# Kernel tuning notes

Measured on AMD Instinct MI355X. Metric: run time of the kernel, lower is better.

Reference implementation:

```python
import jax, jax.numpy as jnp
import numpy as np

EPS = 0.0  # GIN epsilon (train_eps=False)

def setup_inputs() -> dict:
    key = jax.random.key(0)
    k_x, k_e, k_w1, k_w2 = jax.random.split(key, 4)
    N, E, D = 100000, 625000, 128
    x = jax.random.normal(k_x, (N, D), dtype=jnp.float32)
    edge_index = jax.random.randint(k_e, (2, E), 0, N, dtype=jnp.int32)
    s = 1.0 / np.sqrt(D)
    W1 = jax.random.normal(k_w1, (D, D), dtype=jnp.float32) * s
    b1 = jnp.zeros((D,), dtype=jnp.float32)
    W2 = jax.random.normal(k_w2, (D, D), dtype=jnp.float32) * s
    b2 = jnp.zeros((D,), dtype=jnp.float32)
    return {"x": x, "edge_index": edge_index, "W1": W1, "b1": b1, "W2": W2, "b2": b2}

def reference(x, edge_index, W1, b1, W2, b2):
    # GINConv: out_i = MLP((1+eps)*x_i + sum_{j in N(i)} x_j)
    src = edge_index[0]
    dst = edge_index[1]
    agg = jax.ops.segment_sum(x[src], dst, num_segments=x.shape[0])  # [N, D]
    h = (1.0 + EPS) * x + agg
    # MLP: Linear -> ReLU -> Dropout(eval: identity) -> Linear
    h = jax.nn.relu(h @ W1.T + b1)
    h = h @ W2.T + b2
    # outer activation; outer dropout is identity in eval
    return jax.nn.relu(h)
```

## Files before the change

### kernel.cpp

```cpp
#include <hip/hip_runtime.h>


#define D 128
#define HLD 136
#define KSLOT 32
#define CSTR 32

typedef __attribute__((ext_vector_type(8))) short bf16x8;
typedef __attribute__((ext_vector_type(4))) float f32x4;

__device__ __forceinline__ short f2bf(float f) {
    union { float f; unsigned u; } v; v.f = f;
    unsigned r = v.u + 0x7fffu + ((v.u >> 16) & 1u);
    return (short)(r >> 16);
}
__device__ __forceinline__ float bflo(unsigned u) {
    union { unsigned u; float f; } v; v.u = u << 16; return v.f;
}
__device__ __forceinline__ float bfhi(unsigned u) {
    union { unsigned u; float f; } v; v.u = u & 0xffff0000u; return v.f;
}
__device__ __forceinline__ unsigned pack2(float a, float b) {
    return ((unsigned)(unsigned short)f2bf(a)) | (((unsigned)(unsigned short)f2bf(b)) << 16);
}

__global__ __launch_bounds__(256) void convert_fill(const float4* __restrict__ x4,
                                                    unsigned short* __restrict__ xb,
                                                    const int* __restrict__ ei,
                                                    int* __restrict__ cnt,
                                                    int* __restrict__ bucket,
                                                    int nConv, int nConvBlocks, int E) {
    if ((int)blockIdx.x < nConvBlocks) {
        int t = blockIdx.x * 256 + threadIdx.x;
        if (t < nConv) {
            float4 a = x4[2 * t], b = x4[2 * t + 1];
            bf16x8 r;
            r[0] = f2bf(a.x); r[1] = f2bf(a.y); r[2] = f2bf(a.z); r[3] = f2bf(a.w);
            r[4] = f2bf(b.x); r[5] = f2bf(b.y); r[6] = f2bf(b.z); r[7] = f2bf(b.w);
            ((bf16x8*)xb)[t] = r;
        }
    } else {
        int t4 = ((int)blockIdx.x - nConvBlocks) * 256 + threadIdx.x;
        int E4 = E >> 2;
        if (t4 < E4) {
            const int4* ei4 = (const int4*)ei;
            int4 s = ei4[t4];
            int4 d = ei4[E4 + t4];
            int sl;
            sl = atomicAdd(&cnt[d.x * CSTR], 1); if (sl < KSLOT) bucket[d.x * KSLOT + sl] = s.x;
            sl = atomicAdd(&cnt[d.y * CSTR], 1); if (sl < KSLOT) bucket[d.y * KSLOT + sl] = s.y;
            sl = atomicAdd(&cnt[d.z * CSTR], 1); if (sl < KSLOT) bucket[d.z * KSLOT + sl] = s.z;
            sl = atomicAdd(&cnt[d.w * CSTR], 1); if (sl < KSLOT) bucket[d.w * KSLOT + sl] = s.w;
        }
    }
}

__global__ __launch_bounds__(256) void gather_kernel(const uint4* __restrict__ xb4,
                                                     const int* __restrict__ cnt,
                                                     const int* __restrict__ bucket,
                                                     uint4* __restrict__ h04, int N) {
    int g = blockIdx.x * 256 + threadIdx.x;
    int node = g >> 4;
    if (node >= N) return;
    int lane = g & 15;
    int deg = cnt[node * CSTR];
    deg = deg < KSLOT ? deg : KSLOT;
    const int bb = node * KSLOT;

    uint4 sv = xb4[node * 16 + lane];
    float a0 = bflo(sv.x), a1 = bfhi(sv.x), a2 = bflo(sv.y), a3 = bfhi(sv.y);
    float a4 = bflo(sv.z), a5 = bfhi(sv.z), a6 = bflo(sv.w), a7 = bfhi(sv.w);

    int e = 0;
    for (; e + 3 < deg; e += 4) {
        int s0 = bucket[bb + e], s1 = bucket[bb + e + 1];
        int s2 = bucket[bb + e + 2], s3 = bucket[bb + e + 3];
        uint4 p0 = xb4[s0 * 16 + lane];
        uint4 p1 = xb4[s1 * 16 + lane];
        uint4 p2 = xb4[s2 * 16 + lane];
        uint4 p3 = xb4[s3 * 16 + lane];
        a0 += bflo(p0.x) + bflo(p1.x) + bflo(p2.x) + bflo(p3.x);
        a1 += bfhi(p0.x) + bfhi(p1.x) + bfhi(p2.x) + bfhi(p3.x);
        a2 += bflo(p0.y) + bflo(p1.y) + bflo(p2.y) + bflo(p3.y);
        a3 += bfhi(p0.y) + bfhi(p1.y) + bfhi(p2.y) + bfhi(p3.y);
        a4 += bflo(p0.z) + bflo(p1.z) + bflo(p2.z) + bflo(p3.z);
        a5 += bfhi(p0.z) + bfhi(p1.z) + bfhi(p2.z) + bfhi(p3.z);
        a6 += bflo(p0.w) + bflo(p1.w) + bflo(p2.w) + bflo(p3.w);
        a7 += bfhi(p0.w) + bfhi(p1.w) + bfhi(p2.w) + bfhi(p3.w);
    }
    for (; e < deg; ++e) {
        uint4 p = xb4[bucket[bb + e] * 16 + lane];
        a0 += bflo(p.x); a1 += bfhi(p.x); a2 += bflo(p.y); a3 += bfhi(p.y);
        a4 += bflo(p.z); a5 += bfhi(p.z); a6 += bflo(p.w); a7 += bfhi(p.w);
    }
    uint4 r;
    r.x = pack2(a0, a1);
    r.y = pack2(a2, a3);
    r.z = pack2(a4, a5);
    r.w = pack2(a6, a7);
    h04[node * 16 + lane] = r;
}

__global__ __launch_bounds__(512) void mlp_fused(const short* __restrict__ h0,
                                                 const float* __restrict__ W1,
                                                 const float* __restrict__ b1,
                                                 const float* __restrict__ W2,
                                                 const float* __restrict__ b2,
                                                 float* __restrict__ out, int N) {
    __shared__ short W1l[D * HLD];
    __shared__ short W2l[D * HLD];
    __shared__ short h1l[D * HLD];

    {
        const float4* W14 = (const float4*)W1;
        const float4* W24 = (const float4*)W2;
        for (int idx = threadIdx.x; idx < D * (D / 4); idx += 512) {
            int n = idx >> 5;
            int k4 = idx & 31;
            float4 w = W14[idx];
            short* dp = &W1l[n * HLD + k4 * 4];
            dp[0] = f2bf(w.x); dp[1] = f2bf(w.y); dp[2] = f2bf(w.z); dp[3] = f2bf(w.w);
            w = W24[idx];
            dp = &W2l[n * HLD + k4 * 4];
            dp[0] = f2bf(w.x); dp[1] = f2bf(w.y); dp[2] = f2bf(w.z); dp[3] = f2bf(w.w);
        }
    }
    __syncthreads();

    const int wave = threadIdx.x >> 6;
    const int lane = threadIdx.x & 63;
    const int m = lane & 15;
    const int quad = lane >> 4;
    const int tiles = (N + 127) / 128;

    for (int t = blockIdx.x; t < tiles; t += gridDim.x) {
        const int r0 = t * 128 + wave * 16;
        const int arow = r0 + m;

        bf16x8 afrag[4];
        if (arow < N) {
#pragma unroll
            for (int ks = 0; ks < 4; ++ks)
                afrag[ks] = *(const bf16x8*)&h0[(long long)arow * D + ks * 32 + quad * 8];
        } else {
#pragma unroll
            for (int ks = 0; ks < 4; ++ks) afrag[ks] = (bf16x8)(short)0;
        }

        f32x4 acc[8];
#pragma unroll
        for (int jt = 0; jt < 8; ++jt) acc[jt] = (f32x4)0.0f;
#pragma unroll
        for (int jt = 0; jt < 8; ++jt) {
#pragma unroll
            for (int ks = 0; ks < 4; ++ks) {
                bf16x8 b = *(const bf16x8*)&W1l[(jt * 16 + m) * HLD + ks * 32 + quad * 8];
                acc[jt] = __builtin_amdgcn_mfma_f32_16x16x32_bf16(afrag[ks], b, acc[jt], 0, 0, 0);
            }
        }

#pragma unroll
        for (int jt = 0; jt < 8; ++jt) {
            int col = jt * 16 + m;
            float bv = b1[col];
#pragma unroll
            for (int i = 0; i < 4; ++i) {
                float v = acc[jt][i] + bv;
                v = v > 0.0f ? v : 0.0f;
                h1l[(wave * 16 + quad * 4 + i) * HLD + col] = f2bf(v);
            }
        }

        bf16x8 a2[4];
#pragma unroll
        for (int ks = 0; ks < 4; ++ks)
            a2[ks] = *(const bf16x8*)&h1l[(wave * 16 + m) * HLD + ks * 32 + quad * 8];

        f32x4 acc2[8];
#pragma unroll
        for (int jt = 0; jt < 8; ++jt) acc2[jt] = (f32x4)0.0f;
#pragma unroll
        for (int jt = 0; jt < 8; ++jt) {
#pragma unroll
            for (int ks = 0; ks < 4; ++ks) {
                bf16x8 b = *(const bf16x8*)&W2l[(jt * 16 + m) * HLD + ks * 32 + quad * 8];
                acc2[jt] = __builtin_amdgcn_mfma_f32_16x16x32_bf16(a2[ks], b, acc2[jt], 0, 0, 0);
            }
        }

#pragma unroll
        for (int jt = 0; jt < 8; ++jt) {
            int col = jt * 16 + m;
            float bv = b2[col];
#pragma unroll
            for (int i = 0; i < 4; ++i) {
                int row = r0 + quad * 4 + i;
                if (row < N) {
                    float v = acc2[jt][i] + bv;
                    v = v > 0.0f ? v : 0.0f;
                    out[(long long)row * D + col] = v;
                }
            }
        }
    }
}

extern "C" void kernel_launch(void* const* d_in, const int* in_sizes, int n_in,
                              void* d_out, int out_size, void* d_ws, size_t ws_size,
                              hipStream_t stream) {
    const float* x  = (const float*)d_in[0];
    const int*   ei = (const int*)d_in[1];
    const float* W1 = (const float*)d_in[2];
    const float* b1 = (const float*)d_in[3];
    const float* W2 = (const float*)d_in[4];
    const float* b2 = (const float*)d_in[5];
    float* out = (float*)d_out;

    const int N = in_sizes[0] / D;
    const int E = in_sizes[1] / 2;

    unsigned short* h0 = (unsigned short*)d_ws;
    unsigned short* xb = h0 + (size_t)N * D;
    int* cnt    = (int*)(xb + (size_t)N * D);
    int* bucket = cnt + (size_t)N * CSTR;

    hipMemsetAsync(cnt, 0, (size_t)N * CSTR * sizeof(int), stream);

    {
        int nConv = N * (D / 8);
        int nConvBlocks = (nConv + 255) / 256;
        int nFillBlocks = ((E >> 2) + 255) / 256;
        convert_fill<<<nConvBlocks + nFillBlocks, 256, 0, stream>>>(
            (const float4*)x, xb, ei, cnt, bucket, nConv, nConvBlocks, E);
    }

    {
        long long thr = (long long)N * 16;
        gather_kernel<<<(int)((thr + 255) / 256), 256, 0, stream>>>(
            (const uint4*)xb, cnt, bucket, (uint4*)h0, N);
    }

    mlp_fused<<<256, 512, 0, stream>>>((const short*)h0, W1, b1, W2, b2, out, N);
}
```

Baseline: 198.0 us.

## Chunk MLP layer fusion through small LDS, reorder fill blocks, double MLP grid

The MLP kernel now computes the first layer in 32-column chunks and feeds each chunk straight into the second-layer MFMAs through a small per-wave LDS buffer. This replaces the full 128x136 h1 tile, shrinking LDS use so more blocks can be resident, and the grid doubles to 512 blocks with a 4-waves-per-EU launch bound. Biases are hoisted into registers and output stores become nontemporal. The edge-fill part of convert_fill now runs first in block order and handles 8 edges per thread. The risks are register pressure from the occupancy hint and extra LDS round trips per chunk.

```diff
diff --git a/kernel.cpp b/kernel.cpp
--- a/kernel.cpp
+++ b/kernel.cpp
@@ -3,6 +3,7 @@
 
 #define D 128
 #define HLD 136
+#define CPIT 40
 #define KSLOT 32
 #define CSTR 32
 
@@ -29,28 +30,33 @@
                                                     const int* __restrict__ ei,
                                                     int* __restrict__ cnt,
                                                     int* __restrict__ bucket,
-                                                    int nConv, int nConvBlocks, int E) {
-    if ((int)blockIdx.x < nConvBlocks) {
-        int t = blockIdx.x * 256 + threadIdx.x;
+                                                    int nConv, int nFillBlocks, int E) {
+    if ((int)blockIdx.x < nFillBlocks) {
+        int t8 = blockIdx.x * 256 + threadIdx.x;
+        int E8 = E >> 3;
+        if (t8 < E8) {
+            const int4* ei4 = (const int4*)ei;
+            int E4 = E >> 2;
+            int4 s0 = ei4[2 * t8],      s1 = ei4[2 * t8 + 1];
+            int4 d0 = ei4[E4 + 2 * t8], d1 = ei4[E4 + 2 * t8 + 1];
+            int sl;
+            sl = atomicAdd(&cnt[d0.x * CSTR], 1); if (sl < KSLOT) bucket[d0.x * KSLOT + sl] = s0.x;
+            sl = atomicAdd(&cnt[d0.y * CSTR], 1); if (sl < KSLOT) bucket[d0.y * KSLOT + sl] = s0.y;
+            sl = atomicAdd(&cnt[d0.z * CSTR], 1); if (sl < KSLOT) bucket[d0.z * KSLOT + sl] = s0.z;
+            sl = atomicAdd(&cnt[d0.w * CSTR], 1); if (sl < KSLOT) bucket[d0.w * KSLOT + sl] = s0.w;
+            sl = atomicAdd(&cnt[d1.x * CSTR], 1); if (sl < KSLOT) bucket[d1.x * KSLOT + sl] = s1.x;
+            sl = atomicAdd(&cnt[d1.y * CSTR], 1); if (sl < KSLOT) bucket[d1.y * KSLOT + sl] = s1.y;
+            sl = atomicAdd(&cnt[d1.z * CSTR], 1); if (sl < KSLOT) bucket[d1.z * KSLOT + sl] = s1.z;
+            sl = atomicAdd(&cnt[d1.w * CSTR], 1); if (sl < KSLOT) bucket[d1.w * KSLOT + sl] = s1.w;
+        }
+    } else {
+        int t = ((int)blockIdx.x - nFillBlocks) * 256 + threadIdx.x;
         if (t < nConv) {
             float4 a = x4[2 * t], b = x4[2 * t + 1];
             bf16x8 r;
             r[0] = f2bf(a.x); r[1] = f2bf(a.y); r[2] = f2bf(a.z); r[3] = f2bf(a.w);
             r[4] = f2bf(b.x); r[5] = f2bf(b.y); r[6] = f2bf(b.z); r[7] = f2bf(b.w);
             ((bf16x8*)xb)[t] = r;
-        }
-    } else {
-        int t4 = ((int)blockIdx.x - nConvBlocks) * 256 + threadIdx.x;
-        int E4 = E >> 2;
-        if (t4 < E4) {
-            const int4* ei4 = (const int4*)ei;
-            int4 s = ei4[t4];
-            int4 d = ei4[E4 + t4];
-            int sl;
-            sl = atomicAdd(&cnt[d.x * CSTR], 1); if (sl < KSLOT) bucket[d.x * KSLOT + sl] = s.x;
-            sl = atomicAdd(&cnt[d.y * CSTR], 1); if (sl < KSLOT) bucket[d.y * KSLOT + sl] = s.y;
-            sl = atomicAdd(&cnt[d.z * CSTR], 1); if (sl < KSLOT) bucket[d.z * KSLOT + sl] = s.z;
-            sl = atomicAdd(&cnt[d.w * CSTR], 1); if (sl < KSLOT) bucket[d.w * KSLOT + sl] = s.w;
         }
     }
 }
@@ -101,15 +107,15 @@
     h04[node * 16 + lane] = r;
 }
 
-__global__ __launch_bounds__(512) void mlp_fused(const short* __restrict__ h0,
-                                                 const float* __restrict__ W1,
-                                                 const float* __restrict__ b1,
-                                                 const float* __restrict__ W2,
-                                                 const float* __restrict__ b2,
-                                                 float* __restrict__ out, int N) {
+__global__ __launch_bounds__(512, 4) void mlp_fused(const short* __restrict__ h0,
+                                                    const float* __restrict__ W1,
+                                                    const float* __restrict__ b1,
+                                                    const float* __restrict__ W2,
+                                                    const float* __restrict__ b2,
+                                                    float* __restrict__ out, int N) {
     __shared__ short W1l[D * HLD];
     __shared__ short W2l[D * HLD];
-    __shared__ short h1l[D * HLD];
+    __shared__ short chunk[8 * 16 * CPIT];
 
     {
         const float4* W14 = (const float4*)W1;
@@ -132,6 +138,11 @@
     const int m = lane & 15;
     const int quad = lane >> 4;
     const int tiles = (N + 127) / 128;
+    short* ch = &chunk[wave * 16 * CPIT];
+
+    float b1r[8], b2r[8];
+#pragma unroll
+    for (int j = 0; j < 8; ++j) { b1r[j] = b1[j * 16 + m]; b2r[j] = b2[j * 16 + m]; }
 
     for (int t = blockIdx.x; t < tiles; t += gridDim.x) {
         const int r0 = t * 128 + wave * 16;
@@ -147,58 +158,53 @@
             for (int ks = 0; ks < 4; ++ks) afrag[ks] = (bf16x8)(short)0;
         }
 
-        f32x4 acc[8];
-#pragma unroll
-        for (int jt = 0; jt < 8; ++jt) acc[jt] = (f32x4)0.0f;
-#pragma unroll
-        for (int jt = 0; jt < 8; ++jt) {
-#pragma unroll
-            for (int ks = 0; ks < 4; ++ks) {
-                bf16x8 b = *(const bf16x8*)&W1l[(jt * 16 + m) * HLD + ks * 32 + quad * 8];
-                acc[jt] = __builtin_amdgcn_mfma_f32_16x16x32_bf16(afrag[ks], b, acc[jt], 0, 0, 0);
-            }
-        }
-
-#pragma unroll
-        for (int jt = 0; jt < 8; ++jt) {
-            int col = jt * 16 + m;
-            float bv = b1[col];
-#pragma unroll
-            for (int i = 0; i < 4; ++i) {
-                float v = acc[jt][i] + bv;
-                v = v > 0.0f ? v : 0.0f;
-                h1l[(wave * 16 + quad * 4 + i) * HLD + col] = f2bf(v);
-            }
-        }
-
-        bf16x8 a2[4];
-#pragma unroll
-        for (int ks = 0; ks < 4; ++ks)
-            a2[ks] = *(const bf16x8*)&h1l[(wave * 16 + m) * HLD + ks * 32 + quad * 8];
-
         f32x4 acc2[8];
 #pragma unroll
         for (int jt = 0; jt < 8; ++jt) acc2[jt] = (f32x4)0.0f;
-#pragma unroll
-        for (int jt = 0; jt < 8; ++jt) {
-#pragma unroll
-            for (int ks = 0; ks < 4; ++ks) {
-                bf16x8 b = *(const bf16x8*)&W2l[(jt * 16 + m) * HLD + ks * 32 + quad * 8];
-                acc2[jt] = __builtin_amdgcn_mfma_f32_16x16x32_bf16(a2[ks], b, acc2[jt], 0, 0, 0);
-            }
-        }
-
-#pragma unroll
-        for (int jt = 0; jt < 8; ++jt) {
-            int col = jt * 16 + m;
-            float bv = b2[col];
+
+#pragma unroll
+        for (int ks2 = 0; ks2 < 4; ++ks2) {
+            f32x4 acc1[2];
+            acc1[0] = (f32x4)0.0f;
+            acc1[1] = (f32x4)0.0f;
+#pragma unroll
+            for (int half = 0; half < 2; ++half) {
+                int jt = 2 * ks2 + half;
+#pragma unroll
+                for (int ks = 0; ks < 4; ++ks) {
+                    bf16x8 b = *(const bf16x8*)&W1l[(jt * 16 + m) * HLD + ks * 32 + quad * 8];
+                    acc1[half] = __builtin_amdgcn_mfma_f32_16x16x32_bf16(afrag[ks], b, acc1[half], 0, 0, 0);
+                }
+            }
+#pragma unroll
+            for (int half = 0; half < 2; ++half) {
+                float bv = b1r[2 * ks2 + half];
+#pragma unroll
+                for (int i = 0; i < 4; ++i) {
+                    float v = acc1[half][i] + bv;
+                    v = v > 0.0f ? v : 0.0f;
+                    ch[(quad * 4 + i) * CPIT + half * 16 + m] = f2bf(v);
+                }
+            }
+            bf16x8 a2 = *(const bf16x8*)&ch[m * CPIT + quad * 8];
+#pragma unroll
+            for (int jt2 = 0; jt2 < 8; ++jt2) {
+                bf16x8 b = *(const bf16x8*)&W2l[(jt2 * 16 + m) * HLD + ks2 * 32 + quad * 8];
+                acc2[jt2] = __builtin_amdgcn_mfma_f32_16x16x32_bf16(a2, b, acc2[jt2], 0, 0, 0);
+            }
+        }
+
+#pragma unroll
+        for (int jt2 = 0; jt2 < 8; ++jt2) {
+            int col = jt2 * 16 + m;
+            float bv = b2r[jt2];
 #pragma unroll
             for (int i = 0; i < 4; ++i) {
                 int row = r0 + quad * 4 + i;
                 if (row < N) {
-                    float v = acc2[jt][i] + bv;
+                    float v = acc2[jt2][i] + bv;
                     v = v > 0.0f ? v : 0.0f;
-                    out[(long long)row * D + col] = v;
+                    __builtin_nontemporal_store(v, &out[(long long)row * D + col]);
                 }
             }
         }
@@ -229,9 +235,9 @@
     {
         int nConv = N * (D / 8);
         int nConvBlocks = (nConv + 255) / 256;
-        int nFillBlocks = ((E >> 2) + 255) / 256;
-        convert_fill<<<nConvBlocks + nFillBlocks, 256, 0, stream>>>(
-            (const float4*)x, xb, ei, cnt, bucket, nConv, nConvBlocks, E);
+        int nFillBlocks = ((E >> 3) + 255) / 256;
+        convert_fill<<<nFillBlocks + nConvBlocks, 256, 0, stream>>>(
+            (const float4*)x, xb, ei, cnt, bucket, nConv, nFillBlocks, E);
     }
 
     {
@@ -240,5 +246,5 @@
             (const uint4*)xb, cnt, bucket, (uint4*)h0, N);
     }
 
-    mlp_fused<<<256, 512, 0, stream>>>((const short*)h0, W1, b1, W2, b2, out, N);
-}
+    mlp_fused<<<512, 512, 0, stream>>>((const short*)h0, W1, b1, W2, b2, out, N);
+}
```

After: 193.0 us. -2.5%, faster.
